# Optimization experiments

Measured on AMD Instinct MI355X. Metric: run time of the kernel, lower is better.

Reference implementation:

```python
import jax, jax.numpy as jnp
import numpy as np

B, T, C = 4, 4096, 1024


def setup_inputs() -> dict:
    key = jax.random.key(0)
    ks = jax.random.split(key, 5)
    s = 1.0 / np.sqrt(C)
    x = jax.random.normal(ks[0], (B, T, C), dtype=jnp.float32)
    Wq = jax.random.normal(ks[1], (C, C), dtype=jnp.float32) * s
    Wk = jax.random.normal(ks[2], (C, C), dtype=jnp.float32) * s
    Wv = jax.random.normal(ks[3], (C, C), dtype=jnp.float32) * s
    Wo = jax.random.normal(ks[4], (C, C), dtype=jnp.float32) * s
    bo = jnp.zeros((C,), dtype=jnp.float32)
    return {"x": x, "Wq": Wq, "Wk": Wk, "Wv": Wv, "Wo": Wo, "bo": bo}


def reference(x, Wq, Wk, Wv, Wo, bo):
    # Single-head SDPA with causal additive mask; scale = 1/sqrt(C)
    q = jnp.einsum('btc,dc->btd', x, Wq)
    k = jnp.einsum('btc,dc->btd', x, Wk)
    v = jnp.einsum('btc,dc->btd', x, Wv)
    scale = 1.0 / jnp.sqrt(jnp.asarray(C, dtype=x.dtype))
    scores = jnp.einsum('btd,bsd->bts', q, k) * scale  # (B, T, T)
    t = scores.shape[1]
    causal = jnp.tril(jnp.ones((t, t), dtype=bool))
    scores = jnp.where(causal[None, :, :], scores, jnp.asarray(-jnp.inf, dtype=scores.dtype))
    attn = jax.nn.softmax(scores, axis=-1)
    out = jnp.einsum('bts,bsd->btd', attn, v)
    return jnp.einsum('btd,ed->bte', out, Wo) + bo
```

## Files before the change

### kernel.cpp

```cpp
#include <hip/hip_runtime.h>

typedef __bf16 bf16;
typedef __bf16 bf16x4 __attribute__((ext_vector_type(4)));
typedef __bf16 bf16x8 __attribute__((ext_vector_type(8)));
typedef float  f32x4  __attribute__((ext_vector_type(4)));

#define BM 128
#define BN 128
#define BK 32

__device__ __forceinline__ void async_copy16(const void* g, void* l) {
    __builtin_amdgcn_global_load_lds(
        (__attribute__((address_space(1))) void*)(g),
        (__attribute__((address_space(3))) void*)(l),
        16, 0, 0);
}

__global__ __launch_bounds__(256)
void gemm_nt(const bf16* __restrict__ A, int lda, size_t az,
             const bf16* __restrict__ B, int ldb, size_t bz,
             void* __restrict__ C0, void* __restrict__ C1, void* __restrict__ C2,
             int ldc, size_t cz,
             int M, int N, int K, float alpha,
             const float* __restrict__ bias,
             const float* __restrict__ row_scale, int rsz,
             int out_bf16, int qkv_mode, int causal_skip, int kcap, int row_off)
{
    int z  = blockIdx.z;
    int m0 = blockIdx.y * BM;
    int n0 = blockIdx.x * BN;
    if (causal_skip && n0 > row_off + m0 + BM - 1) return;
    int Keff = kcap ? min(K, row_off + m0 + BM) : K;
    A += (size_t)z * az;
    B += (size_t)z * bz;

    __shared__ __attribute__((aligned(16))) bf16 As[BM * BK];
    __shared__ __attribute__((aligned(16))) bf16 Bs[BN * BK];

    int tid  = threadIdx.x;
    int lane = tid & 63;
    int q    = lane >> 4;
    int r    = lane & 15;
    int wave = tid >> 6;
    int wm   = (wave >> 1) * 64;
    int wn   = (wave & 1) * 64;
    int sw   = (r >> 1) & 3;
    int gsw  = ((tid & 3) ^ ((tid >> 3) & 3)) * 8;

    f32x4 acc[4][4];
#pragma unroll
    for (int i = 0; i < 4; i++)
#pragma unroll
        for (int j = 0; j < 4; j++) acc[i][j] = (f32x4){0.f, 0.f, 0.f, 0.f};

    const bf16* Ag = A + (size_t)(m0 + (tid >> 2)) * lda + gsw;
    const bf16* Bg = B + (size_t)(n0 + (tid >> 2)) * ldb + gsw;
    char* lAs = (char*)As + tid * 16;
    char* lBs = (char*)Bs + tid * 16;
    size_t astep = (size_t)64 * lda;
    size_t bstep = (size_t)64 * ldb;

    for (int k0 = 0; k0 < Keff; k0 += BK) {
        async_copy16(Ag + k0,         lAs);
        async_copy16(Ag + k0 + astep, lAs + 4096);
        async_copy16(Bg + k0,         lBs);
        async_copy16(Bg + k0 + bstep, lBs + 4096);
        asm volatile("s_waitcnt vmcnt(0)" ::: "memory");
        __syncthreads();

        bf16x8 av[4], bv[4];
#pragma unroll
        for (int mi = 0; mi < 4; mi++)
            av[mi] = *(const bf16x8*)&As[(wm + mi * 16 + r) * BK + (q ^ sw) * 8];
#pragma unroll
        for (int ni = 0; ni < 4; ni++)
            bv[ni] = *(const bf16x8*)&Bs[(wn + ni * 16 + r) * BK + (q ^ sw) * 8];
#pragma unroll
        for (int mi = 0; mi < 4; mi++)
#pragma unroll
            for (int ni = 0; ni < 4; ni++)
                acc[mi][ni] = __builtin_amdgcn_mfma_f32_16x16x32_bf16(
                    av[mi], bv[ni], acc[mi][ni], 0, 0, 0);
        __syncthreads();
    }

    const float* rs = row_scale ? row_scale + (size_t)z * rsz : nullptr;
    void* Cb = C0;
    if (qkv_mode) { int sel = n0 >> 10; Cb = sel == 0 ? C0 : (sel == 1 ? C1 : C2); }
#pragma unroll
    for (int mi = 0; mi < 4; mi++) {
#pragma unroll
        for (int ni = 0; ni < 4; ni++) {
#pragma unroll
            for (int j = 0; j < 4; j++) {
                int row = m0 + wm + mi * 16 + q * 4 + j;
                int col = n0 + wn + ni * 16 + r;
                if (qkv_mode) col &= 1023;
                float v = acc[mi][ni][j] * alpha;
                if (rs)   v *= rs[row];
                if (bias) v += bias[col];
                if (out_bf16) ((bf16*)Cb + (size_t)z * cz)[(size_t)row * ldc + col] = (bf16)v;
                else          ((float*)Cb + (size_t)z * cz)[(size_t)row * ldc + col] = v;
            }
        }
    }
}

__global__ __launch_bounds__(256)
void softmax_causal(bf16* __restrict__ S, float* __restrict__ inv_l,
                    int T, int toff, int chunk)
{
    int tr = blockIdx.x, z = blockIdx.y;
    int t  = toff + tr;
    int L  = t + 1;
    int Lw = ((t >> 7) + 1) << 7;
    bf16* row = S + ((size_t)z * chunk + tr) * T;
    int tid = threadIdx.x;
    __shared__ float buf[4096];
    __shared__ float red[4];

    for (int s = tid * 8; s < Lw; s += 2048) {
        bf16x8 v = *(const bf16x8*)(row + s);
#pragma unroll
        for (int i = 0; i < 8; i++)
            buf[s + i] = (s + i < L) ? (float)v[i] : -3.0e38f;
    }
    __syncthreads();

    float m = -3.0e38f;
    for (int s = tid; s < Lw; s += 256) m = fmaxf(m, buf[s]);
#pragma unroll
    for (int off = 32; off > 0; off >>= 1) m = fmaxf(m, __shfl_down(m, off, 64));
    if ((tid & 63) == 0) red[tid >> 6] = m;
    __syncthreads();
    m = fmaxf(fmaxf(red[0], red[1]), fmaxf(red[2], red[3]));
    __syncthreads();

    float sum = 0.f;
    for (int s = tid * 8; s < Lw; s += 2048) {
        bf16x8 o;
#pragma unroll
        for (int i = 0; i < 8; i++) {
            float e = __expf(buf[s + i] - m);
            sum += e;
            o[i] = (bf16)e;
        }
        *(bf16x8*)(row + s) = o;
    }
#pragma unroll
    for (int off = 32; off > 0; off >>= 1) sum += __shfl_down(sum, off, 64);
    if ((tid & 63) == 0) red[tid >> 6] = sum;
    __syncthreads();
    if (tid == 0) inv_l[(size_t)z * chunk + tr] = 1.0f / (red[0] + red[1] + red[2] + red[3]);
}

__global__ __launch_bounds__(256)
void transpose64(const bf16* __restrict__ V, bf16* __restrict__ VT, int T, int C)
{
    __shared__ bf16 tile[64][65];
    int b  = blockIdx.z;
    int s0 = blockIdx.x * 64, d0 = blockIdx.y * 64;
    const bf16* Vb  = V  + (size_t)b * T * C;
    bf16*       VTb = VT + (size_t)b * T * C;
    int tx = threadIdx.x & 63, ty = threadIdx.x >> 6;
#pragma unroll
    for (int i = 0; i < 64; i += 4)
        tile[ty + i][tx] = Vb[(size_t)(s0 + ty + i) * C + d0 + tx];
    __syncthreads();
#pragma unroll
    for (int i = 0; i < 64; i += 4)
        VTb[(size_t)(d0 + ty + i) * T + s0 + tx] = tile[tx][ty + i];
}

__global__ void cvt_f32_bf16(const float4* __restrict__ in, bf16x4* __restrict__ out, int n4)
{
    int i = blockIdx.x * blockDim.x + threadIdx.x;
    int stride = gridDim.x * blockDim.x;
    for (; i < n4; i += stride) {
        float4 v = in[i];
        bf16x4 o = { (bf16)v.x, (bf16)v.y, (bf16)v.z, (bf16)v.w };
        out[i] = o;
    }
}

extern "C" void kernel_launch(void* const* d_in, const int* in_sizes, int n_in,
                              void* d_out, int out_size, void* d_ws, size_t ws_size,
                              hipStream_t stream)
{
    const int B = 4, T = 4096, C = 1024, M = B * T;
    const float* x  = (const float*)d_in[0];
    const float* Wq = (const float*)d_in[1];
    const float* Wk = (const float*)d_in[2];
    const float* Wv = (const float*)d_in[3];
    const float* Wo = (const float*)d_in[4];
    const float* bo = (const float*)d_in[5];
    float* out = (float*)d_out;

    char* ws = (char*)d_ws;
    size_t off = 0;
    auto alloc = [&](size_t bytes) -> char* {
        char* p = ws + off;
        off += (bytes + 255) & ~(size_t)255;
        return p;
    };
    bf16* Wcat = (bf16*)alloc((size_t)3 * C * C * 2);
    bf16* Wob  = (bf16*)alloc((size_t)C * C * 2);
    bf16* Qb   = (bf16*)alloc((size_t)M * C * 2);
    bf16* Kb   = (bf16*)alloc((size_t)M * C * 2);
    bf16* VT   = (bf16*)alloc((size_t)M * C * 2);
    bf16* Ob   = (bf16*)alloc((size_t)M * C * 2);

    int chunk = T;
    while (chunk > 1024) {
        size_t need = off + (((size_t)B * chunk * T * 2 + 255) & ~(size_t)255)
                          + (((size_t)B * chunk * 4 + 255) & ~(size_t)255);
        if (need <= ws_size) break;
        chunk >>= 1;
    }
    bf16*  S     = (bf16*)alloc((size_t)B * chunk * T * 2);
    float* inv_l = (float*)alloc((size_t)B * chunk * 4);
    bf16*  xb    = S;

    dim3 blk(256);

    cvt_f32_bf16<<<dim3(4096), blk, 0, stream>>>((const float4*)x,  (bf16x4*)xb, M * C / 4);
    cvt_f32_bf16<<<dim3(1024), blk, 0, stream>>>((const float4*)Wq, (bf16x4*)(Wcat),             C * C / 4);
    cvt_f32_bf16<<<dim3(1024), blk, 0, stream>>>((const float4*)Wk, (bf16x4*)(Wcat + C * C),     C * C / 4);
    cvt_f32_bf16<<<dim3(1024), blk, 0, stream>>>((const float4*)Wv, (bf16x4*)(Wcat + 2 * C * C), C * C / 4);
    cvt_f32_bf16<<<dim3(1024), blk, 0, stream>>>((const float4*)Wo, (bf16x4*)Wob, C * C / 4);

    gemm_nt<<<dim3(3 * C / BN, M / BM, 1), blk, 0, stream>>>(
        xb, C, 0, Wcat, C, 0, Qb, Kb, Ob, C, 0, M, 3 * C, C, 1.f,
        nullptr, nullptr, 0, 1, 1, 0, 0, 0);
    transpose64<<<dim3(T / 64, C / 64, B), blk, 0, stream>>>(Ob, VT, T, C);

    const float scale = 0.03125f;
    for (int toff = 0; toff < T; toff += chunk) {
        gemm_nt<<<dim3(T / BN, chunk / BM, B), blk, 0, stream>>>(
            Qb + (size_t)toff * C, C, (size_t)T * C,
            Kb, C, (size_t)T * C,
            S, nullptr, nullptr, T, (size_t)chunk * T,
            chunk, T, C, scale,
            nullptr, nullptr, 0, 1, 0, 1, 0, toff);
        softmax_causal<<<dim3(chunk, B), blk, 0, stream>>>(S, inv_l, T, toff, chunk);
        gemm_nt<<<dim3(C / BN, chunk / BM, B), blk, 0, stream>>>(
            S, T, (size_t)chunk * T,
            VT, T, (size_t)T * C,
            Ob + (size_t)toff * C, nullptr, nullptr, C, (size_t)T * C,
            chunk, C, T, 1.f,
            nullptr, inv_l, chunk, 1, 0, 0, 1, toff);
    }

    gemm_nt<<<dim3(C / BN, M / BM, 1), blk, 0, stream>>>(
        Ob, C, 0, Wob, C, 0, out, nullptr, nullptr, C, 0, M, C, C, 1.f,
        bo, nullptr, 0, 0, 0, 0, 0, 0);
}
```

Measured before the change: 768.7 us.

## Alias workspace buffers to fit full score matrix and reverse causal row order

Reorganizes workspace allocation so the full T×T score buffer fits by aliasing the attention output onto Q and the V staging buffer into the score region, removing the chunked loop when memory allows. Adds a rev_m flag so causal GEMMs launch the heaviest row blocks first for better load balance. Risks depend on buffer aliasing lifetimes being correct and on the workspace size.

After: 716.7 us. 1.07x faster.

```diff
diff --git a/kernel.cpp b/kernel.cpp
--- a/kernel.cpp
+++ b/kernel.cpp
@@ -24,10 +24,12 @@
              int M, int N, int K, float alpha,
              const float* __restrict__ bias,
              const float* __restrict__ row_scale, int rsz,
-             int out_bf16, int qkv_mode, int causal_skip, int kcap, int row_off)
+             int out_bf16, int qkv_mode, int causal_skip, int kcap,
+             int row_off, int rev_m)
 {
     int z  = blockIdx.z;
-    int m0 = blockIdx.y * BM;
+    int by = rev_m ? (gridDim.y - 1 - blockIdx.y) : blockIdx.y;
+    int m0 = by * BM;
     int n0 = blockIdx.x * BN;
     if (causal_skip && n0 > row_off + m0 + BM - 1) return;
     int Keff = kcap ? min(K, row_off + m0 + BM) : K;
@@ -208,18 +210,35 @@
     bf16* Qb   = (bf16*)alloc((size_t)M * C * 2);
     bf16* Kb   = (bf16*)alloc((size_t)M * C * 2);
     bf16* VT   = (bf16*)alloc((size_t)M * C * 2);
-    bf16* Ob   = (bf16*)alloc((size_t)M * C * 2);
-
+
+    size_t base = off;
     int chunk = T;
-    while (chunk > 1024) {
-        size_t need = off + (((size_t)B * chunk * T * 2 + 255) & ~(size_t)255)
-                          + (((size_t)B * chunk * 4 + 255) & ~(size_t)255);
-        if (need <= ws_size) break;
-        chunk >>= 1;
-    }
-    bf16*  S     = (bf16*)alloc((size_t)B * chunk * T * 2);
-    float* inv_l = (float*)alloc((size_t)B * chunk * 4);
-    bf16*  xb    = S;
+    bf16 *S, *xb, *Vtmp, *Ob;
+    float* inv_l;
+    {
+        size_t need = base + (((size_t)B * T * T * 2 + 255) & ~(size_t)255)
+                           + (((size_t)B * T * 4 + 255) & ~(size_t)255);
+        if (need <= ws_size) {
+            S     = (bf16*)alloc((size_t)B * T * T * 2);
+            inv_l = (float*)alloc((size_t)B * T * 4);
+            xb    = S;
+            Vtmp  = S + (size_t)M * C;
+            Ob    = Qb;
+        } else {
+            Ob = (bf16*)alloc((size_t)M * C * 2);
+            chunk = T / 2;
+            while (chunk > 1024) {
+                size_t nd = off + (((size_t)B * chunk * T * 2 + 255) & ~(size_t)255)
+                                + (((size_t)B * chunk * 4 + 255) & ~(size_t)255);
+                if (nd <= ws_size) break;
+                chunk >>= 1;
+            }
+            S     = (bf16*)alloc((size_t)B * chunk * T * 2);
+            inv_l = (float*)alloc((size_t)B * chunk * 4);
+            xb    = S;
+            Vtmp  = Ob;
+        }
+    }
 
     dim3 blk(256);
 
@@ -230,9 +249,9 @@
     cvt_f32_bf16<<<dim3(1024), blk, 0, stream>>>((const float4*)Wo, (bf16x4*)Wob, C * C / 4);
 
     gemm_nt<<<dim3(3 * C / BN, M / BM, 1), blk, 0, stream>>>(
-        xb, C, 0, Wcat, C, 0, Qb, Kb, Ob, C, 0, M, 3 * C, C, 1.f,
-        nullptr, nullptr, 0, 1, 1, 0, 0, 0);
-    transpose64<<<dim3(T / 64, C / 64, B), blk, 0, stream>>>(Ob, VT, T, C);
+        xb, C, 0, Wcat, C, 0, Qb, Kb, Vtmp, C, 0, M, 3 * C, C, 1.f,
+        nullptr, nullptr, 0, 1, 1, 0, 0, 0, 0);
+    transpose64<<<dim3(T / 64, C / 64, B), blk, 0, stream>>>(Vtmp, VT, T, C);
 
     const float scale = 0.03125f;
     for (int toff = 0; toff < T; toff += chunk) {
@@ -241,17 +260,17 @@
             Kb, C, (size_t)T * C,
             S, nullptr, nullptr, T, (size_t)chunk * T,
             chunk, T, C, scale,
-            nullptr, nullptr, 0, 1, 0, 1, 0, toff);
+            nullptr, nullptr, 0, 1, 0, 1, 0, toff, 1);
         softmax_causal<<<dim3(chunk, B), blk, 0, stream>>>(S, inv_l, T, toff, chunk);
         gemm_nt<<<dim3(C / BN, chunk / BM, B), blk, 0, stream>>>(
             S, T, (size_t)chunk * T,
             VT, T, (size_t)T * C,
             Ob + (size_t)toff * C, nullptr, nullptr, C, (size_t)T * C,
             chunk, C, T, 1.f,
-            nullptr, inv_l, chunk, 1, 0, 0, 1, toff);
+            nullptr, inv_l, chunk, 1, 0, 0, 1, toff, 1);
     }
 
     gemm_nt<<<dim3(C / BN, M / BM, 1), blk, 0, stream>>>(
         Ob, C, 0, Wob, C, 0, out, nullptr, nullptr, C, 0, M, C, C, 1.f,
-        bo, nullptr, 0, 0, 0, 0, 0, 0);
-}
+        bo, nullptr, 0, 0, 0, 0, 0, 0, 0);
+}
```
